# Optimization experiments

Measured on AMD Instinct MI355X. Metric: run time of the kernel, lower is better.

The kernel has to match this reference:

```python
import jax, jax.numpy as jnp
import numpy as np

T, B, I, H, K = 200, 2048, 128, 128, 4


def setup_inputs() -> dict:
    key = jax.random.key(0)
    ks = jax.random.split(key, 7)
    inputs = jax.random.normal(ks[0], (T, B, I), jnp.float32)
    lengths = jax.random.randint(ks[1], (B,), 1, T + 1, jnp.int32)
    si = 1.0 / np.sqrt(I)
    sh = 1.0 / np.sqrt(H)
    w0 = jax.random.uniform(ks[2], (H,), jnp.float32, -sh, sh)      # Linear(H,1,bias=False)
    w1_w = jax.random.uniform(ks[3], (H, I), jnp.float32, -si, si)  # Linear(I,H)
    w1_b = jax.random.uniform(ks[4], (H,), jnp.float32, -si, si)
    w2_w = jax.random.uniform(ks[5], (H, I), jnp.float32, -si, si)  # Linear(I,H,bias=False)
    w3_w = jax.random.uniform(ks[6], (H, I), jnp.float32, -si, si)  # Linear(I,H,bias=False)
    return dict(inputs=inputs, lengths=lengths, label_len=4,
                w0=w0, w1_w=w1_w, w1_b=w1_b, w2_w=w2_w, w3_w=w3_w)


def reference(inputs, lengths, label_len, w0, w1_w, w1_b, w2_w, w3_w):
    # inputs: [T, B, I] time-major padded sequences; lengths: [B]
    T_, B_, _ = inputs.shape
    Kl = label_len
    dt = inputs.dtype
    # packed semantics: padded positions are exactly zero
    valid = (jnp.arange(T_)[:, None] < lengths[None, :])  # [T, B]
    x = inputs * valid[..., None].astype(dt)
    x1 = x @ w1_w.T + w1_b                                 # [T, B, H]
    x2 = x @ w2_w.T                                        # [T, B, H]
    # running mean m_s[t] = mean(inputs[:t+1]) (zeros at padding, as in torch)
    m_s = jnp.cumsum(x, axis=0) / jnp.arange(1, T_ + 1, dtype=dt)[:, None, None]
    # labeled timesteps: last min(L, label_len) steps of each sequence
    start = jnp.maximum(lengths - Kl, 0)                   # [B]
    t_lab = start[:, None] + jnp.arange(Kl)[None, :]       # [B, K]
    lab_valid = t_lab < lengths[:, None]                   # [B, K]
    t_c = jnp.minimum(t_lab, T_ - 1)
    b_idx = jnp.arange(B_)[:, None]
    x2_lab = x2[t_c, b_idx]                                # [B, K, H]
    wms_lab = m_s[t_c, b_idx] @ w3_w.T                     # [B, K, H]
    c = x2_lab + wms_lab                                   # [B, K, H]
    # att[b,k,s] = w0 . sigmoid(x1[s,b] + x2[t_k,b] + wms[t_k,b])
    att = jnp.einsum('sbkh,h->bks',
                     jax.nn.sigmoid(x1[:, :, None, :] + c[None, :, :, :]), w0)
    causal = (jnp.arange(T_)[None, None, :] <= t_lab[:, :, None]) & lab_valid[:, :, None]
    att = att * causal.astype(dt)                          # [B, K, T]
    h = jnp.einsum('bks,sbh->bkh', att, x1) + x2_lab       # [B, K, H]
    return h * lab_valid[..., None].astype(dt)
```

## Files before the change

### kernel.cpp

```cpp
#include <hip/hip_runtime.h>
#include <stdint.h>

#define T_DIM 200
#define B_DIM 2048
#define I_DIM 128
#define H_DIM 128
#define TS    16

typedef float  f32x4  __attribute__((ext_vector_type(4)));
typedef __bf16 bf16x8 __attribute__((ext_vector_type(8)));

union BF8 { ushort4 u2[2]; bf16x8 v; };

static __device__ __forceinline__ unsigned short f2bf(float f) {
    union { float f; unsigned u; } c; c.f = f;
    unsigned u = c.u + (0x7FFFu + ((c.u >> 16) & 1u));
    return (unsigned short)(u >> 16);
}
static __device__ __forceinline__ float bf2f(unsigned short s) {
    union { unsigned u; float f; } c; c.u = ((unsigned)s) << 16;
    return c.f;
}
static __device__ __forceinline__ bf16x8 cvt8(const float4 a, const float4 b) {
    BF8 t;
    t.u2[0] = make_ushort4(f2bf(a.x), f2bf(a.y), f2bf(a.z), f2bf(a.w));
    t.u2[1] = make_ushort4(f2bf(b.x), f2bf(b.y), f2bf(b.z), f2bf(b.w));
    return t.v;
}

__global__ __launch_bounds__(256, 4) void fused_kernel(
    const float* __restrict__ x, const int* __restrict__ lengths,
    const float* __restrict__ w0, const float* __restrict__ w1,
    const float* __restrict__ b1, const float* __restrict__ w2,
    const float* __restrict__ w3, float* __restrict__ out)
{
    __shared__ __align__(16) float psum[4][128];
    __shared__ __align__(16) unsigned short axl[4][132];
    __shared__ __align__(16) unsigned short ams[4][132];
    __shared__ __align__(16) float ektL[H_DIM][4];
    __shared__ __align__(16) float attk[2][TS][4];

    const int b    = blockIdx.x;
    const int tid  = threadIdx.x;
    const int lane = tid & 63;
    const int wv   = tid >> 6;
    const int l15  = lane & 15;
    const int quad = lane >> 4;
    const int L     = lengths[b];
    const int start = (L > 4) ? (L - 4) : 0;
    const int nv    = (L < 4) ? L : 4;
    const int hbase = wv * 32;

    if (tid < 128) ((float*)attk)[tid] = 0.f;

    bf16x8 bfr[2][4];
    float  biasr[2], w0r[2];
    #pragma unroll
    for (int nt = 0; nt < 2; ++nt) {
        const int n = hbase + nt * 16 + l15;
        biasr[nt] = b1[n];
        w0r[nt]   = w0[n];
        #pragma unroll
        for (int ks = 0; ks < 4; ++ks) {
            const int kc = ks * 32 + quad * 8;
            bfr[nt][ks] = cvt8(*(const float4*)(w1 + (size_t)n * I_DIM + kc),
                               *(const float4*)(w1 + (size_t)n * I_DIM + kc + 4));
        }
    }

    {
        const int q  = (start + 3) >> 2;
        const int tb = wv * q;
        const int te = (tb + q < start) ? (tb + q) : start;
        const float* xb2 = x + (size_t)b * I_DIM + 2 * lane;
        float s0 = 0.f, s1 = 0.f;
        int t = tb;
        for (; t + 4 <= te; t += 4) {
            const float2 a0 = *(const float2*)(xb2 + (size_t)(t + 0) * (B_DIM * I_DIM));
            const float2 a1 = *(const float2*)(xb2 + (size_t)(t + 1) * (B_DIM * I_DIM));
            const float2 a2 = *(const float2*)(xb2 + (size_t)(t + 2) * (B_DIM * I_DIM));
            const float2 a3 = *(const float2*)(xb2 + (size_t)(t + 3) * (B_DIM * I_DIM));
            s0 += a0.x + a1.x + a2.x + a3.x;
            s1 += a0.y + a1.y + a2.y + a3.y;
        }
        for (; t < te; ++t) {
            const float2 a = *(const float2*)(xb2 + (size_t)t * (B_DIM * I_DIM));
            s0 += a.x; s1 += a.y;
        }
        psum[wv][2 * lane]     = s0;
        psum[wv][2 * lane + 1] = s1;
    }
    __syncthreads();

    if (tid < 128) {
        const int i = tid;
        float p = psum[0][i] + psum[1][i] + psum[2][i] + psum[3][i];
        const float* xi = x + (size_t)b * I_DIM + i;
        const float v0 = xi[(size_t)(start + 0) * (B_DIM * I_DIM)];
        const float v1 = xi[(size_t)(start + 1) * (B_DIM * I_DIM)];
        const float v2 = xi[(size_t)(start + 2) * (B_DIM * I_DIM)];
        const float v3 = xi[(size_t)(start + 3) * (B_DIM * I_DIM)];
        const float p0 = p + v0, p1 = p0 + v1, p2 = p1 + v2, p3 = p2 + v3;
        axl[0][i] = f2bf(v0); axl[1][i] = f2bf(v1);
        axl[2][i] = f2bf(v2); axl[3][i] = f2bf(v3);
        ams[0][i] = f2bf(p0 / (float)(start + 1));
        ams[1][i] = f2bf(p1 / (float)(start + 2));
        ams[2][i] = f2bf(p2 / (float)(start + 3));
        ams[3][i] = f2bf(p3 / (float)(start + 4));
    }
    __syncthreads();

    f32x4 x2lr[2];
    #pragma unroll
    for (int nt = 0; nt < 2; ++nt) {
        const int n = hbase + nt * 16 + l15;
        f32x4 c1 = (f32x4){0.f, 0.f, 0.f, 0.f};
        f32x4 c2 = (f32x4){0.f, 0.f, 0.f, 0.f};
        #pragma unroll
        for (int ks = 0; ks < 4; ++ks) {
            const int kc = ks * 32 + quad * 8;
            const bf16x8 a1 = *(const bf16x8*)&axl[l15 & 3][kc];
            const bf16x8 a2 = *(const bf16x8*)&ams[l15 & 3][kc];
            const bf16x8 b2 = cvt8(*(const float4*)(w2 + (size_t)n * I_DIM + kc),
                                   *(const float4*)(w2 + (size_t)n * I_DIM + kc + 4));
            const bf16x8 b3 = cvt8(*(const float4*)(w3 + (size_t)n * I_DIM + kc),
                                   *(const float4*)(w3 + (size_t)n * I_DIM + kc + 4));
            c1 = __builtin_amdgcn_mfma_f32_16x16x32_bf16(a1, b2, c1, 0, 0, 0);
            c2 = __builtin_amdgcn_mfma_f32_16x16x32_bf16(a2, b3, c2, 0, 0, 0);
        }
        x2lr[nt] = c1;
        if (quad == 0) {
            f32x4 e;
            #pragma unroll
            for (int k = 0; k < 4; ++k)
                e[k] = __builtin_amdgcn_exp2f(-1.44269504f * (c1[k] + c2[k]));
            *(f32x4*)&ektL[n][0] = e;
        }
    }
    __syncthreads();

    f32x4 ektr[2];
    #pragma unroll
    for (int nt = 0; nt < 2; ++nt)
        ektr[nt] = *(const f32x4*)&ektL[hbase + nt * 16 + l15][0];

    float hacc[2][4];
    #pragma unroll
    for (int nt = 0; nt < 2; ++nt)
        #pragma unroll
        for (int k = 0; k < 4; ++k) hacc[nt][k] = 0.f;

    int parity = 0;
    for (int t0 = 0; t0 < L; t0 += TS, parity ^= 1) {
        const int  row  = t0 + l15;
        const bool vrow = row < L;
        const int  ra   = vrow ? row : (L - 1);
        const float* xr = x + ((size_t)ra * B_DIM + b) * I_DIM + quad * 8;
        bf16x8 afr[4];
        #pragma unroll
        for (int ks = 0; ks < 4; ++ks) {
            float4 p0 = *(const float4*)(xr + ks * 32);
            float4 p1 = *(const float4*)(xr + ks * 32 + 4);
            if (!vrow) { p0 = make_float4(0, 0, 0, 0); p1 = make_float4(0, 0, 0, 0); }
            afr[ks] = cvt8(p0, p1);
        }

        float x1c[2][4];
        #pragma unroll
        for (int nt = 0; nt < 2; ++nt) {
            f32x4 acc = (f32x4){0.f, 0.f, 0.f, 0.f};
            #pragma unroll
            for (int ks = 0; ks < 4; ++ks)
                acc = __builtin_amdgcn_mfma_f32_16x16x32_bf16(afr[ks], bfr[nt][ks], acc, 0, 0, 0);
            #pragma unroll
            for (int r = 0; r < 4; ++r) x1c[nt][r] = acc[r] + biasr[nt];
        }

        float part[4][4];
        #pragma unroll
        for (int r = 0; r < 4; ++r) {
            #pragma unroll
            for (int k = 0; k < 4; ++k) part[r][k] = 0.f;
            #pragma unroll
            for (int nt = 0; nt < 2; ++nt) {
                const float E = __builtin_amdgcn_exp2f(-1.44269504f * x1c[nt][r]);
                #pragma unroll
                for (int k = 0; k < 4; ++k)
                    part[r][k] += w0r[nt] * __builtin_amdgcn_rcpf(1.f + E * ektr[nt][k]);
            }
        }
        #pragma unroll
        for (int m = 1; m <= 8; m <<= 1)
            #pragma unroll
            for (int r = 0; r < 4; ++r)
                #pragma unroll
                for (int k = 0; k < 4; ++k)
                    part[r][k] += __shfl_xor(part[r][k], m);

        if (l15 == 0) {
            #pragma unroll
            for (int r = 0; r < 4; ++r) {
                const int s = t0 + quad * 4 + r;
                #pragma unroll
                for (int k = 0; k < 4; ++k) {
                    const float v = (k < nv && s <= start + k) ? part[r][k] : 0.f;
                    atomicAdd(&attk[parity][quad * 4 + r][k], v);
                }
            }
        }
        __syncthreads();

        #pragma unroll
        for (int r = 0; r < 4; ++r) {
            const f32x4 a4 = *(const f32x4*)&attk[parity][quad * 4 + r][0];
            #pragma unroll
            for (int nt = 0; nt < 2; ++nt)
                #pragma unroll
                for (int k = 0; k < 4; ++k)
                    hacc[nt][k] += a4[k] * x1c[nt][r];
        }
        if (tid < 64) ((float*)&attk[parity ^ 1][0][0])[tid] = 0.f;
        __syncthreads();
    }

    #pragma unroll
    for (int nt = 0; nt < 2; ++nt)
        #pragma unroll
        for (int k = 0; k < 4; ++k) {
            float v = hacc[nt][k];
            v += __shfl_xor(v, 16);
            v += __shfl_xor(v, 32);
            hacc[nt][k] = v;
        }
    if (quad == 0) {
        #pragma unroll
        for (int nt = 0; nt < 2; ++nt) {
            const int h = hbase + nt * 16 + l15;
            #pragma unroll
            for (int k = 0; k < 4; ++k)
                out[((size_t)b * 4 + k) * H_DIM + h] =
                    (k < nv) ? (hacc[nt][k] + x2lr[nt][k]) : 0.f;
        }
    }
}

extern "C" void kernel_launch(void* const* d_in, const int* in_sizes, int n_in,
                              void* d_out, int out_size, void* d_ws, size_t ws_size,
                              hipStream_t stream) {
    (void)in_sizes; (void)n_in; (void)out_size; (void)d_ws; (void)ws_size;
    const float* x       = (const float*)d_in[0];
    const int*   lengths = (const int*)d_in[1];
    const float* w0 = (const float*)d_in[3];
    const float* w1 = (const float*)d_in[4];
    const float* b1 = (const float*)d_in[5];
    const float* w2 = (const float*)d_in[6];
    const float* w3 = (const float*)d_in[7];
    float* out = (float*)d_out;

    fused_kernel<<<dim3(B_DIM), 256, 0, stream>>>(x, lengths, w0, w1, b1, w2, w3, out);
}
```

Baseline: 388.4 us.

## Split fused per-batch kernel into four kernels parallel over time chunks

Replaces the single kernel, which ran one block per batch and looped serially over time tiles, with four launches. The new kernels convert W1 to bf16 once, compute prefix sums in parallel per time chunk, compute the label-side terms per batch, and handle each 16-step time tile in its own block. Tile results are accumulated into the output with global atomics. This exposes far more parallelism across the ragged sequence lengths, at the cost of extra launches, workspace traffic, a second read of x, and nondeterministic float atomic accumulation.

```diff
diff --git a/kernel.cpp b/kernel.cpp
--- a/kernel.cpp
+++ b/kernel.cpp
@@ -6,6 +6,7 @@
 #define I_DIM 128
 #define H_DIM 128
 #define TS    16
+#define NC    13
 
 typedef float  f32x4  __attribute__((ext_vector_type(4)));
 typedef __bf16 bf16x8 __attribute__((ext_vector_type(8)));
@@ -16,10 +17,6 @@
     union { float f; unsigned u; } c; c.f = f;
     unsigned u = c.u + (0x7FFFu + ((c.u >> 16) & 1u));
     return (unsigned short)(u >> 16);
-}
-static __device__ __forceinline__ float bf2f(unsigned short s) {
-    union { unsigned u; float f; } c; c.u = ((unsigned)s) << 16;
-    return c.f;
 }
 static __device__ __forceinline__ bf16x8 cvt8(const float4 a, const float4 b) {
     BF8 t;
@@ -28,73 +25,60 @@
     return t.v;
 }
 
-__global__ __launch_bounds__(256, 4) void fused_kernel(
+__global__ __launch_bounds__(256) void k0_cvt(
+    const float* __restrict__ w1, unsigned short* __restrict__ w1b)
+{
+    const int idx = (blockIdx.x * 256 + threadIdx.x) * 4;
+    const float4 v = *(const float4*)(w1 + idx);
+    *(ushort4*)(w1b + idx) = make_ushort4(f2bf(v.x), f2bf(v.y), f2bf(v.z), f2bf(v.w));
+}
+
+__global__ __launch_bounds__(256) void k1_sums(
     const float* __restrict__ x, const int* __restrict__ lengths,
-    const float* __restrict__ w0, const float* __restrict__ w1,
-    const float* __restrict__ b1, const float* __restrict__ w2,
-    const float* __restrict__ w3, float* __restrict__ out)
-{
-    __shared__ __align__(16) float psum[4][128];
-    __shared__ __align__(16) unsigned short axl[4][132];
-    __shared__ __align__(16) unsigned short ams[4][132];
-    __shared__ __align__(16) float ektL[H_DIM][4];
-    __shared__ __align__(16) float attk[2][TS][4];
-
-    const int b    = blockIdx.x;
-    const int tid  = threadIdx.x;
-    const int lane = tid & 63;
-    const int wv   = tid >> 6;
-    const int l15  = lane & 15;
-    const int quad = lane >> 4;
+    float* __restrict__ part)
+{
+    const int c = blockIdx.x, b = blockIdx.y;
+    const int L = lengths[b];
+    const int start = (L > 4) ? (L - 4) : 0;
+    const int t0 = c * TS;
+    if (t0 >= start) return;
+
+    __shared__ float red[128];
+    const int i = threadIdx.x & 127;
+    const int g = threadIdx.x >> 7;
+    const float* xp = x + (size_t)b * I_DIM + i;
+    float s = 0.f;
+    #pragma unroll
+    for (int r = 0; r < 8; ++r) {
+        const int t = t0 + g * 8 + r;
+        if (t < start) s += xp[(size_t)t * (B_DIM * I_DIM)];
+    }
+    if (g == 1) red[i] = s;
+    __syncthreads();
+    if (g == 0) part[((size_t)b * NC + c) * I_DIM + i] = s + red[i];
+}
+
+__global__ __launch_bounds__(256) void k2_label(
+    const float* __restrict__ x, const int* __restrict__ lengths,
+    const float* __restrict__ w2, const float* __restrict__ w3,
+    const float* __restrict__ part, float* __restrict__ ektw,
+    float* __restrict__ out)
+{
+    __shared__ __align__(16) unsigned short axl[4][136];
+    __shared__ __align__(16) unsigned short ams[4][136];
+
+    const int b   = blockIdx.x;
+    const int tid = threadIdx.x;
     const int L     = lengths[b];
     const int start = (L > 4) ? (L - 4) : 0;
     const int nv    = (L < 4) ? L : 4;
-    const int hbase = wv * 32;
-
-    if (tid < 128) ((float*)attk)[tid] = 0.f;
-
-    bf16x8 bfr[2][4];
-    float  biasr[2], w0r[2];
-    #pragma unroll
-    for (int nt = 0; nt < 2; ++nt) {
-        const int n = hbase + nt * 16 + l15;
-        biasr[nt] = b1[n];
-        w0r[nt]   = w0[n];
-        #pragma unroll
-        for (int ks = 0; ks < 4; ++ks) {
-            const int kc = ks * 32 + quad * 8;
-            bfr[nt][ks] = cvt8(*(const float4*)(w1 + (size_t)n * I_DIM + kc),
-                               *(const float4*)(w1 + (size_t)n * I_DIM + kc + 4));
-        }
-    }
-
-    {
-        const int q  = (start + 3) >> 2;
-        const int tb = wv * q;
-        const int te = (tb + q < start) ? (tb + q) : start;
-        const float* xb2 = x + (size_t)b * I_DIM + 2 * lane;
-        float s0 = 0.f, s1 = 0.f;
-        int t = tb;
-        for (; t + 4 <= te; t += 4) {
-            const float2 a0 = *(const float2*)(xb2 + (size_t)(t + 0) * (B_DIM * I_DIM));
-            const float2 a1 = *(const float2*)(xb2 + (size_t)(t + 1) * (B_DIM * I_DIM));
-            const float2 a2 = *(const float2*)(xb2 + (size_t)(t + 2) * (B_DIM * I_DIM));
-            const float2 a3 = *(const float2*)(xb2 + (size_t)(t + 3) * (B_DIM * I_DIM));
-            s0 += a0.x + a1.x + a2.x + a3.x;
-            s1 += a0.y + a1.y + a2.y + a3.y;
-        }
-        for (; t < te; ++t) {
-            const float2 a = *(const float2*)(xb2 + (size_t)t * (B_DIM * I_DIM));
-            s0 += a.x; s1 += a.y;
-        }
-        psum[wv][2 * lane]     = s0;
-        psum[wv][2 * lane + 1] = s1;
-    }
-    __syncthreads();
 
     if (tid < 128) {
         const int i = tid;
-        float p = psum[0][i] + psum[1][i] + psum[2][i] + psum[3][i];
+        float p = 0.f;
+        const int ncs = (start + TS - 1) / TS;
+        for (int cc = 0; cc < ncs; ++cc)
+            p += part[((size_t)b * NC + cc) * I_DIM + i];
         const float* xi = x + (size_t)b * I_DIM + i;
         const float v0 = xi[(size_t)(start + 0) * (B_DIM * I_DIM)];
         const float v1 = xi[(size_t)(start + 1) * (B_DIM * I_DIM)];
@@ -110,10 +94,10 @@
     }
     __syncthreads();
 
-    f32x4 x2lr[2];
-    #pragma unroll
-    for (int nt = 0; nt < 2; ++nt) {
-        const int n = hbase + nt * 16 + l15;
+    const int lane = tid & 63, wv = tid >> 6, l15 = lane & 15, quad = lane >> 4;
+    #pragma unroll
+    for (int nt = 0; nt < 2; ++nt) {
+        const int n = wv * 32 + nt * 16 + l15;
         f32x4 c1 = (f32x4){0.f, 0.f, 0.f, 0.f};
         f32x4 c2 = (f32x4){0.f, 0.f, 0.f, 0.f};
         #pragma unroll
@@ -128,118 +112,142 @@
             c1 = __builtin_amdgcn_mfma_f32_16x16x32_bf16(a1, b2, c1, 0, 0, 0);
             c2 = __builtin_amdgcn_mfma_f32_16x16x32_bf16(a2, b3, c2, 0, 0, 0);
         }
-        x2lr[nt] = c1;
         if (quad == 0) {
             f32x4 e;
             #pragma unroll
-            for (int k = 0; k < 4; ++k)
-                e[k] = __builtin_amdgcn_exp2f(-1.44269504f * (c1[k] + c2[k]));
-            *(f32x4*)&ektL[n][0] = e;
-        }
-    }
-    __syncthreads();
-
-    f32x4 ektr[2];
+            for (int r = 0; r < 4; ++r) {
+                e[r] = __builtin_amdgcn_exp2f(-1.44269504f * (c1[r] + c2[r]));
+                out[((size_t)b * 4 + r) * H_DIM + n] = (r < nv) ? c1[r] : 0.f;
+            }
+            *(f32x4*)(ektw + ((size_t)b * H_DIM + n) * 4) = e;
+        }
+    }
+}
+
+__global__ __launch_bounds__(256) void k3_tile(
+    const float* __restrict__ x, const int* __restrict__ lengths,
+    const unsigned short* __restrict__ w1b, const float* __restrict__ b1,
+    const float* __restrict__ w0, const float* __restrict__ ektw,
+    float* __restrict__ out)
+{
+    const int c = blockIdx.x, b = blockIdx.y;
+    const int L  = lengths[b];
+    const int t0 = c * TS;
+    if (t0 >= L) return;
+    const int start = (L > 4) ? (L - 4) : 0;
+    const int nv    = (L < 4) ? L : 4;
+
+    __shared__ __align__(16) unsigned short xs[TS][136];
+    __shared__ __align__(16) float ektLS[H_DIM][4];
+    __shared__ __align__(16) float attp[4][TS][4];
+
+    const int tid  = threadIdx.x;
+    const int lane = tid & 63;
+    const int wv   = tid >> 6;
+    const int l15  = lane & 15;
+    const int quad = lane >> 4;
+    const int hb   = wv * 32;
+
+    {
+        const int r = tid >> 4, seg = tid & 15;
+        const int t = t0 + r;
+        ushort4 wa = make_ushort4(0, 0, 0, 0), wb = make_ushort4(0, 0, 0, 0);
+        if (t < L) {
+            const float* xr = x + ((size_t)t * B_DIM + b) * I_DIM + seg * 8;
+            const float4 p0 = *(const float4*)(xr);
+            const float4 p1 = *(const float4*)(xr + 4);
+            wa = make_ushort4(f2bf(p0.x), f2bf(p0.y), f2bf(p0.z), f2bf(p0.w));
+            wb = make_ushort4(f2bf(p1.x), f2bf(p1.y), f2bf(p1.z), f2bf(p1.w));
+        }
+        *(ushort4*)&xs[r][seg * 8]     = wa;
+        *(ushort4*)&xs[r][seg * 8 + 4] = wb;
+    }
+    if (tid < 128)
+        *(f32x4*)&ektLS[tid][0] = *(const f32x4*)(ektw + ((size_t)b * H_DIM + tid) * 4);
+    __syncthreads();
+
+    bf16x8 afr[2][4];
     #pragma unroll
     for (int nt = 0; nt < 2; ++nt)
-        ektr[nt] = *(const f32x4*)&ektL[hbase + nt * 16 + l15][0];
-
-    float hacc[2][4];
-    #pragma unroll
-    for (int nt = 0; nt < 2; ++nt)
-        #pragma unroll
-        for (int k = 0; k < 4; ++k) hacc[nt][k] = 0.f;
-
-    int parity = 0;
-    for (int t0 = 0; t0 < L; t0 += TS, parity ^= 1) {
-        const int  row  = t0 + l15;
-        const bool vrow = row < L;
-        const int  ra   = vrow ? row : (L - 1);
-        const float* xr = x + ((size_t)ra * B_DIM + b) * I_DIM + quad * 8;
-        bf16x8 afr[4];
-        #pragma unroll
-        for (int ks = 0; ks < 4; ++ks) {
-            float4 p0 = *(const float4*)(xr + ks * 32);
-            float4 p1 = *(const float4*)(xr + ks * 32 + 4);
-            if (!vrow) { p0 = make_float4(0, 0, 0, 0); p1 = make_float4(0, 0, 0, 0); }
-            afr[ks] = cvt8(p0, p1);
-        }
-
-        float x1c[2][4];
-        #pragma unroll
-        for (int nt = 0; nt < 2; ++nt) {
-            f32x4 acc = (f32x4){0.f, 0.f, 0.f, 0.f};
-            #pragma unroll
-            for (int ks = 0; ks < 4; ++ks)
-                acc = __builtin_amdgcn_mfma_f32_16x16x32_bf16(afr[ks], bfr[nt][ks], acc, 0, 0, 0);
-            #pragma unroll
-            for (int r = 0; r < 4; ++r) x1c[nt][r] = acc[r] + biasr[nt];
-        }
-
-        float part[4][4];
+        #pragma unroll
+        for (int ks = 0; ks < 4; ++ks)
+            afr[nt][ks] = *(const bf16x8*)(
+                w1b + (size_t)(hb + nt * 16 + l15) * I_DIM + ks * 32 + quad * 8);
+    bf16x8 xfr[4];
+    #pragma unroll
+    for (int ks = 0; ks < 4; ++ks)
+        xfr[ks] = *(const bf16x8*)&xs[l15][ks * 32 + quad * 8];
+
+    float  x1c[2][4];
+    float4 bias4[2], w04[2];
+    #pragma unroll
+    for (int nt = 0; nt < 2; ++nt) {
+        f32x4 acc = (f32x4){0.f, 0.f, 0.f, 0.f};
+        #pragma unroll
+        for (int ks = 0; ks < 4; ++ks)
+            acc = __builtin_amdgcn_mfma_f32_16x16x32_bf16(afr[nt][ks], xfr[ks], acc, 0, 0, 0);
+        bias4[nt] = *(const float4*)(b1 + hb + nt * 16 + quad * 4);
+        w04[nt]   = *(const float4*)(w0 + hb + nt * 16 + quad * 4);
+        const float* bp = (const float*)&bias4[nt];
+        #pragma unroll
+        for (int r = 0; r < 4; ++r) x1c[nt][r] = acc[r] + bp[r];
+    }
+
+    float att[4] = {0.f, 0.f, 0.f, 0.f};
+    #pragma unroll
+    for (int nt = 0; nt < 2; ++nt) {
+        const float* wp = (const float*)&w04[nt];
         #pragma unroll
         for (int r = 0; r < 4; ++r) {
-            #pragma unroll
-            for (int k = 0; k < 4; ++k) part[r][k] = 0.f;
-            #pragma unroll
-            for (int nt = 0; nt < 2; ++nt) {
-                const float E = __builtin_amdgcn_exp2f(-1.44269504f * x1c[nt][r]);
-                #pragma unroll
-                for (int k = 0; k < 4; ++k)
-                    part[r][k] += w0r[nt] * __builtin_amdgcn_rcpf(1.f + E * ektr[nt][k]);
-            }
-        }
-        #pragma unroll
-        for (int m = 1; m <= 8; m <<= 1)
-            #pragma unroll
-            for (int r = 0; r < 4; ++r)
-                #pragma unroll
-                for (int k = 0; k < 4; ++k)
-                    part[r][k] += __shfl_xor(part[r][k], m);
-
-        if (l15 == 0) {
-            #pragma unroll
-            for (int r = 0; r < 4; ++r) {
-                const int s = t0 + quad * 4 + r;
-                #pragma unroll
-                for (int k = 0; k < 4; ++k) {
-                    const float v = (k < nv && s <= start + k) ? part[r][k] : 0.f;
-                    atomicAdd(&attk[parity][quad * 4 + r][k], v);
-                }
-            }
-        }
-        __syncthreads();
-
-        #pragma unroll
-        for (int r = 0; r < 4; ++r) {
-            const f32x4 a4 = *(const f32x4*)&attk[parity][quad * 4 + r][0];
-            #pragma unroll
-            for (int nt = 0; nt < 2; ++nt)
-                #pragma unroll
-                for (int k = 0; k < 4; ++k)
-                    hacc[nt][k] += a4[k] * x1c[nt][r];
-        }
-        if (tid < 64) ((float*)&attk[parity ^ 1][0][0])[tid] = 0.f;
-        __syncthreads();
-    }
-
-    #pragma unroll
-    for (int nt = 0; nt < 2; ++nt)
-        #pragma unroll
-        for (int k = 0; k < 4; ++k) {
-            float v = hacc[nt][k];
-            v += __shfl_xor(v, 16);
-            v += __shfl_xor(v, 32);
-            hacc[nt][k] = v;
-        }
-    if (quad == 0) {
-        #pragma unroll
-        for (int nt = 0; nt < 2; ++nt) {
-            const int h = hbase + nt * 16 + l15;
+            const f32x4 ekv = *(const f32x4*)&ektLS[hb + nt * 16 + quad * 4 + r][0];
+            const float E  = __builtin_amdgcn_exp2f(-1.44269504f * x1c[nt][r]);
+            const float wh = wp[r];
             #pragma unroll
             for (int k = 0; k < 4; ++k)
-                out[((size_t)b * 4 + k) * H_DIM + h] =
-                    (k < nv) ? (hacc[nt][k] + x2lr[nt][k]) : 0.f;
+                att[k] += wh * __builtin_amdgcn_rcpf(1.f + E * ekv[k]);
+        }
+    }
+    #pragma unroll
+    for (int k = 0; k < 4; ++k) {
+        att[k] += __shfl_xor(att[k], 16);
+        att[k] += __shfl_xor(att[k], 32);
+    }
+    if (quad == 0)
+        *(f32x4*)&attp[wv][l15][0] = (f32x4){att[0], att[1], att[2], att[3]};
+    __syncthreads();
+
+    f32x4 as = *(const f32x4*)&attp[0][l15][0];
+    as += *(const f32x4*)&attp[1][l15][0];
+    as += *(const f32x4*)&attp[2][l15][0];
+    as += *(const f32x4*)&attp[3][l15][0];
+    const int s = t0 + l15;
+    float am[4];
+    #pragma unroll
+    for (int k = 0; k < 4; ++k)
+        am[k] = (k < nv && s <= start + k) ? as[k] : 0.f;
+
+    #pragma unroll
+    for (int nt = 0; nt < 2; ++nt) {
+        #pragma unroll
+        for (int r = 0; r < 4; ++r) {
+            float v0 = am[0] * x1c[nt][r];
+            float v1 = am[1] * x1c[nt][r];
+            float v2 = am[2] * x1c[nt][r];
+            float v3 = am[3] * x1c[nt][r];
+            #pragma unroll
+            for (int m = 1; m <= 8; m <<= 1) {
+                v0 += __shfl_xor(v0, m);
+                v1 += __shfl_xor(v1, m);
+                v2 += __shfl_xor(v2, m);
+                v3 += __shfl_xor(v3, m);
+            }
+            if (l15 == 0) {
+                const int h = hb + nt * 16 + quad * 4 + r;
+                atomicAdd(&out[((size_t)b * 4 + 0) * H_DIM + h], v0);
+                atomicAdd(&out[((size_t)b * 4 + 1) * H_DIM + h], v1);
+                atomicAdd(&out[((size_t)b * 4 + 2) * H_DIM + h], v2);
+                atomicAdd(&out[((size_t)b * 4 + 3) * H_DIM + h], v3);
+            }
         }
     }
 }
@@ -247,7 +255,7 @@
 extern "C" void kernel_launch(void* const* d_in, const int* in_sizes, int n_in,
                               void* d_out, int out_size, void* d_ws, size_t ws_size,
                               hipStream_t stream) {
-    (void)in_sizes; (void)n_in; (void)out_size; (void)d_ws; (void)ws_size;
+    (void)in_sizes; (void)n_in; (void)out_size; (void)ws_size;
     const float* x       = (const float*)d_in[0];
     const int*   lengths = (const int*)d_in[1];
     const float* w0 = (const float*)d_in[3];
@@ -257,5 +265,12 @@
     const float* w3 = (const float*)d_in[7];
     float* out = (float*)d_out;
 
-    fused_kernel<<<dim3(B_DIM), 256, 0, stream>>>(x, lengths, w0, w1, b1, w2, w3, out);
-}
+    unsigned short* w1bf = (unsigned short*)d_ws;
+    float* part = (float*)((char*)d_ws + 32768);
+    float* ektw = (float*)((char*)d_ws + 32768 + (size_t)B_DIM * NC * I_DIM * 4);
+
+    k0_cvt <<<dim3(16),         256, 0, stream>>>(w1, w1bf);
+    k1_sums<<<dim3(NC, B_DIM),  256, 0, stream>>>(x, lengths, part);
+    k2_label<<<dim3(B_DIM),     256, 0, stream>>>(x, lengths, w2, w3, part, ektw, out);
+    k3_tile<<<dim3(NC, B_DIM),  256, 0, stream>>>(x, lengths, w1bf, b1, w0, ektw, out);
+}
```

New measurement: 433.5 us. 1.12x slower.
